# Kernel tuning notes

Measured on AMD Instinct MI355X. Metric: run time of the kernel, lower is better.

## Reference

```python
import jax, jax.numpy as jnp
import numpy as np

N = 100000      # nodes
E = 1600000     # edges (before self-loops)
IN_DIM = 128
HID = 32
HEADS = 4
EMB = 128
SLOPE = 0.2     # PyG GATConv default negative_slope


def setup_inputs() -> dict:
    key = jax.random.key(0)
    ks = jax.random.split(key, 16)
    def glorot(k, shape):
        fan_in = shape[0] if len(shape) > 1 else shape[-1]
        return jax.random.normal(k, shape, jnp.float32) * (1.0 / np.sqrt(fan_in))
    x = jax.random.normal(ks[0], (N, IN_DIM), jnp.float32)
    edge_index = jax.random.randint(ks[1], (2, E), 0, N)
    return {
        "x": x,
        "edge_index": edge_index,
        # layer 1: in_dim -> hidden (heads=4, concat)
        "W1": glorot(ks[2], (IN_DIM, HEADS * HID)),
        "att_src1": glorot(ks[3], (HEADS, HID)),
        "att_dst1": glorot(ks[4], (HEADS, HID)),
        "b1": jnp.zeros((HEADS * HID,), jnp.float32),
        # layer 2: hidden*heads -> hidden (heads=4, concat)
        "W2": glorot(ks[5], (HEADS * HID, HEADS * HID)),
        "att_src2": glorot(ks[6], (HEADS, HID)),
        "att_dst2": glorot(ks[7], (HEADS, HID)),
        "b2": jnp.zeros((HEADS * HID,), jnp.float32),
        # layer 3: hidden*heads -> embed (heads=1)
        "W3": glorot(ks[8], (HEADS * HID, EMB)),
        "att_src3": glorot(ks[9], (1, EMB)),
        "att_dst3": glorot(ks[10], (1, EMB)),
        "b3": jnp.zeros((EMB,), jnp.float32),
    }


def gat_conv(x, src, dst, W, att_src, att_dst, b, heads, out_ch):
    """One PyG-style GATConv (concat=True). src/dst already include self-loops."""
    n = x.shape[0]
    h = (x @ W).reshape(n, heads, out_ch)                 # [N,H,C]
    a_s = jnp.einsum('nhc,hc->nh', h, att_src)            # [N,H]
    a_d = jnp.einsum('nhc,hc->nh', h, att_dst)            # [N,H]
    e = jax.nn.leaky_relu(a_s[src] + a_d[dst], SLOPE)     # [E',H]
    # numerically stable softmax over irregular incoming neighborhoods (per dst)
    m = jax.ops.segment_max(e, dst, num_segments=n)       # [N,H]
    ex = jnp.exp(e - m[dst])
    denom = jax.ops.segment_sum(ex, dst, num_segments=n)  # [N,H]
    alpha = ex / denom[dst]                                # [E',H]
    out = jax.ops.segment_sum(h[src] * alpha[:, :, None], dst, num_segments=n)
    return out.reshape(n, heads * out_ch) + b


def reference(x, edge_index, W1, att_src1, att_dst1, b1,
              W2, att_src2, att_dst2, b2, W3, att_src3, att_dst3, b3):
    n = x.shape[0]
    loops = jnp.arange(n, dtype=edge_index.dtype)
    src = jnp.concatenate([edge_index[0], loops])  # PyG add_self_loops=True
    dst = jnp.concatenate([edge_index[1], loops])
    h = gat_conv(x, src, dst, W1, att_src1, att_dst1, b1, HEADS, HID)
    h = jax.nn.elu(h)
    h = gat_conv(h, src, dst, W2, att_src2, att_dst2, b2, HEADS, HID)
    h = jax.nn.elu(h)
    out = gat_conv(h, src, dst, W3, att_src3, att_dst3, b3, 1, EMB)
    return out
```

## Files before the change

### kernel.cpp

```cpp
#include <hip/hip_runtime.h>
#include <hip/hip_fp16.h>
#include <math.h>

#define N_NODES 100000
#define N_EDGES 1600000
#define SLOPE 0.2f

#define BSHIFT 8
#define NB 391
#define CHUNK 8192

typedef _Float16 f16x8 __attribute__((ext_vector_type(8)));
typedef float f32x4 __attribute__((ext_vector_type(4)));

__global__ __launch_bounds__(256) void partA1(const int* __restrict__ ei,
                                              int* __restrict__ bucket_count,
                                              int E, int n) {
  __shared__ int cnt[NB];
  for (int i = threadIdx.x; i < NB; i += 256) cnt[i] = 0;
  __syncthreads();
  int base = blockIdx.x * CHUNK;
  int total = E + n;
  int lim = min(base + CHUNK, total);
  for (int e = base + threadIdx.x; e < lim; e += 256) {
    int d = (e < E) ? ei[E + e] : (e - E);
    atomicAdd(&cnt[d >> BSHIFT], 1);
  }
  __syncthreads();
  for (int i = threadIdx.x; i < NB; i += 256)
    if (cnt[i]) atomicAdd(&bucket_count[i], cnt[i]);
}

__global__ __launch_bounds__(512) void scan_nb(
    const int* __restrict__ bucket_count, int* __restrict__ bucket_base,
    int* __restrict__ bucket_cursor) {
  __shared__ int lds[512];
  int t = threadIdx.x;
  int v = (t < NB) ? bucket_count[t] : 0;
  int x = v;
  lds[t] = x;
  __syncthreads();
  for (int off = 1; off < 512; off <<= 1) {
    int y = (t >= off) ? lds[t - off] : 0;
    __syncthreads();
    x += y;
    lds[t] = x;
    __syncthreads();
  }
  int excl = x - v;
  if (t <= NB) bucket_base[t] = excl;
  if (t < NB) bucket_cursor[t] = excl;
}

__global__ __launch_bounds__(256) void partA2(const int* __restrict__ ei,
                                              int* __restrict__ bucket_cursor,
                                              unsigned* __restrict__ part,
                                              int E, int n) {
  __shared__ int cnt[NB];
  __shared__ int res[NB];
  for (int i = threadIdx.x; i < NB; i += 256) cnt[i] = 0;
  __syncthreads();
  int base = blockIdx.x * CHUNK;
  int total = E + n;
  int lim = min(base + CHUNK, total);
  for (int e = base + threadIdx.x; e < lim; e += 256) {
    int d = (e < E) ? ei[E + e] : (e - E);
    atomicAdd(&cnt[d >> BSHIFT], 1);
  }
  __syncthreads();
  for (int i = threadIdx.x; i < NB; i += 256)
    res[i] = cnt[i] ? atomicAdd(&bucket_cursor[i], cnt[i]) : 0;
  __syncthreads();
  for (int e = base + threadIdx.x; e < lim; e += 256) {
    int s, d;
    if (e < E) { s = ei[e]; d = ei[E + e]; } else { s = d = e - E; }
    int b = d >> BSHIFT;
    int pos = atomicAdd(&res[b], 1);
    part[pos] = ((unsigned)s << BSHIFT) | (unsigned)(d & 255);
  }
}

__global__ __launch_bounds__(256) void passB(const unsigned* __restrict__ part,
                                             const int* __restrict__ bucket_base,
                                             int* __restrict__ row_start,
                                             int* __restrict__ edge_src, int n) {
  __shared__ int cnt[256];
  __shared__ int sc[256];
  __shared__ int loff[256];
  int b = blockIdx.x;
  int t = threadIdx.x;
  int node0 = b << BSHIFT;
  int bstart = bucket_base[b], bend = bucket_base[b + 1];
  cnt[t] = 0;
  __syncthreads();
  for (int i = bstart + t; i < bend; i += 256)
    atomicAdd(&cnt[part[i] & 255], 1);
  __syncthreads();
  int v = cnt[t];
  int x = v;
  sc[t] = x;
  __syncthreads();
  for (int off = 1; off < 256; off <<= 1) {
    int y = (t >= off) ? sc[t - off] : 0;
    __syncthreads();
    x += y;
    sc[t] = x;
    __syncthreads();
  }
  int excl = x - v;
  loff[t] = excl;
  int node = node0 + t;
  if (node < n) row_start[node] = bstart + excl;
  if (b == NB - 1 && t == 0) row_start[n] = bucket_base[NB];
  __syncthreads();
  for (int i = bstart + t; i < bend; i += 256) {
    unsigned p = part[i];
    int dl = p & 255;
    int pos = bstart + atomicAdd(&loff[dl], 1);
    edge_src[pos] = (int)(p >> BSHIFT);
  }
}

__global__ __launch_bounds__(256) void convert_w(
    const float* __restrict__ W1, const float* __restrict__ W2,
    const float* __restrict__ W3, __half* __restrict__ Wt1,
    __half* __restrict__ Wt2, __half* __restrict__ Wt3) {
  int idx = blockIdx.x * 256 + threadIdx.x;
  if (idx >= 3 * 16384) return;
  int mat = idx >> 14;
  int r = idx & 16383;
  int k = r >> 7, col = r & 127;
  const float* W = (mat == 0) ? W1 : (mat == 1) ? W2 : W3;
  __half* Wt = (mat == 0) ? Wt1 : (mat == 1) ? Wt2 : Wt3;
  Wt[col * 128 + k] = __float2half(W[k * 128 + col]);
}

template <int H>
__global__ __launch_bounds__(256) void gemm_att_mfma(
    const float* __restrict__ X, const __half* __restrict__ Wt,
    const float* __restrict__ att_src, const float* __restrict__ att_dst,
    __half* __restrict__ Y, float* __restrict__ a_s, float* __restrict__ a_d,
    int n) {
  __shared__ _Float16 A_lds[64 * 128];
  __shared__ _Float16 B_lds[128 * 128];
  int t = threadIdx.x;
  int r0 = blockIdx.x * 64;

  {
    int row = t >> 2;
    int c0 = (t & 3) * 32;
    const float* xp = X + (size_t)(r0 + row) * 128 + c0;
    bool inb = (r0 + row) < n;
#pragma unroll
    for (int i = 0; i < 8; i++) {
      float4 v;
      if (inb) v = *(const float4*)(xp + i * 4);
      else v = make_float4(0.f, 0.f, 0.f, 0.f);
      union { float2 f; __half2 h2[2]; } u;
      u.h2[0] = __floats2half2_rn(v.x, v.y);
      u.h2[1] = __floats2half2_rn(v.z, v.w);
      *(float2*)&A_lds[row * 128 + c0 + i * 4] = u.f;
    }
  }
  {
    const __half* wp = Wt + t * 64;
#pragma unroll
    for (int i = 0; i < 8; i++)
      *(float4*)&B_lds[t * 64 + i * 8] = *(const float4*)(wp + i * 8);
  }
  __syncthreads();

  int wv = t >> 6, lane = t & 63, quad = lane >> 4, l15 = lane & 15;
  const _Float16* Arow = &A_lds[(wv * 16 + l15) * 128];
  f32x4 acc[8];
#pragma unroll
  for (int ct = 0; ct < 8; ct++) acc[ct] = (f32x4){0.f, 0.f, 0.f, 0.f};

#pragma unroll
  for (int kb = 0; kb < 4; kb++) {
    f16x8 a = *(const f16x8*)(Arow + kb * 32 + quad * 8);
#pragma unroll
    for (int ct = 0; ct < 8; ct++) {
      f16x8 b = *(const f16x8*)(&B_lds[(ct * 16 + l15) * 128 + kb * 32 + quad * 8]);
      acc[ct] = __builtin_amdgcn_mfma_f32_16x16x32_f16(a, b, acc[ct], 0, 0, 0);
    }
  }

  int rbase = r0 + wv * 16 + quad * 4;
#pragma unroll
  for (int reg = 0; reg < 4; reg++) {
    int row = rbase + reg;
    if (row < n) {
#pragma unroll
      for (int ct = 0; ct < 8; ct++)
        Y[(size_t)row * 128 + ct * 16 + l15] = __float2half(acc[ct][reg]);
    }
  }

  float avs[8], avd[8];
#pragma unroll
  for (int ct = 0; ct < 8; ct++) {
    avs[ct] = att_src[ct * 16 + l15];
    avd[ct] = att_dst[ct * 16 + l15];
  }
  if constexpr (H == 4) {
    float ps[4][4], pd_[4][4];
#pragma unroll
    for (int hd = 0; hd < 4; hd++)
#pragma unroll
      for (int reg = 0; reg < 4; reg++) { ps[hd][reg] = 0.f; pd_[hd][reg] = 0.f; }
#pragma unroll
    for (int ct = 0; ct < 8; ct++) {
      int hd = ct >> 1;
#pragma unroll
      for (int reg = 0; reg < 4; reg++) {
        ps[hd][reg] = fmaf(acc[ct][reg], avs[ct], ps[hd][reg]);
        pd_[hd][reg] = fmaf(acc[ct][reg], avd[ct], pd_[hd][reg]);
      }
    }
#pragma unroll
    for (int off = 1; off <= 8; off <<= 1)
#pragma unroll
      for (int hd = 0; hd < 4; hd++)
#pragma unroll
        for (int reg = 0; reg < 4; reg++) {
          ps[hd][reg] += __shfl_xor(ps[hd][reg], off, 64);
          pd_[hd][reg] += __shfl_xor(pd_[hd][reg], off, 64);
        }
#pragma unroll
    for (int hd = 0; hd < 4; hd++)
      if (l15 == hd) {
#pragma unroll
        for (int reg = 0; reg < 4; reg++) {
          int row = rbase + reg;
          if (row < n) {
            a_s[row * 4 + hd] = ps[hd][reg];
            a_d[row * 4 + hd] = pd_[hd][reg];
          }
        }
      }
  } else {
    float ps[4] = {}, pd_[4] = {};
#pragma unroll
    for (int ct = 0; ct < 8; ct++)
#pragma unroll
      for (int reg = 0; reg < 4; reg++) {
        ps[reg] = fmaf(acc[ct][reg], avs[ct], ps[reg]);
        pd_[reg] = fmaf(acc[ct][reg], avd[ct], pd_[reg]);
      }
#pragma unroll
    for (int off = 1; off <= 8; off <<= 1)
#pragma unroll
      for (int reg = 0; reg < 4; reg++) {
        ps[reg] += __shfl_xor(ps[reg], off, 64);
        pd_[reg] += __shfl_xor(pd_[reg], off, 64);
      }
    if (l15 == 0) {
#pragma unroll
      for (int reg = 0; reg < 4; reg++) {
        int row = rbase + reg;
        if (row < n) { a_s[row] = ps[reg]; a_d[row] = pd_[reg]; }
      }
    }
  }
}

template <int H, bool DO_ELU>
__global__ __launch_bounds__(256) void agg_kernel(
    const __half* __restrict__ h, const float* __restrict__ a_s,
    const float* __restrict__ a_d, const int* __restrict__ row_start,
    const int* __restrict__ edge_src, const float* __restrict__ bias,
    float* __restrict__ out, int n) {
  const int C = 128 / H;
  __shared__ float w_lds[4][H * 66];
  __shared__ int sn_lds[4][64];
  int wslot = threadIdx.x >> 6;
  int wid = (blockIdx.x * blockDim.x + threadIdx.x) >> 6;
  int lane = threadIdx.x & 63;
  if (wid >= n) return;
  int start = row_start[wid], end = row_start[wid + 1];
  int deg = end - start;

  float adv[H];
#pragma unroll
  for (int hh = 0; hh < H; hh++) adv[hh] = a_d[wid * H + hh];

  if (deg <= 64) {
    bool valid = lane < deg;
    int sn = valid ? edge_src[start + lane] : 0;
    float e[H];
    if (valid) {
      if constexpr (H == 4) {
        float4 asv = *(const float4*)(a_s + (size_t)sn * 4);
        float t0 = asv.x + adv[0];
        float t1 = asv.y + adv[1];
        float t2 = asv.z + adv[2];
        float t3 = asv.w + adv[3];
        e[0] = t0 >= 0.f ? t0 : SLOPE * t0;
        e[1] = t1 >= 0.f ? t1 : SLOPE * t1;
        e[2] = t2 >= 0.f ? t2 : SLOPE * t2;
        e[3] = t3 >= 0.f ? t3 : SLOPE * t3;
      } else {
        float tt = a_s[sn] + adv[0];
        e[0] = tt >= 0.f ? tt : SLOPE * tt;
      }
    } else {
#pragma unroll
      for (int hh = 0; hh < H; hh++) e[hh] = -1e30f;
    }
    bool small = (deg <= 32);
    float m[H], w[H], s[H];
#pragma unroll
    for (int hh = 0; hh < H; hh++) m[hh] = e[hh];
#pragma unroll
    for (int off = 1; off <= 16; off <<= 1)
#pragma unroll
      for (int hh = 0; hh < H; hh++)
        m[hh] = fmaxf(m[hh], __shfl_xor(m[hh], off, 64));
    if (!small)
#pragma unroll
      for (int hh = 0; hh < H; hh++)
        m[hh] = fmaxf(m[hh], __shfl_xor(m[hh], 32, 64));
#pragma unroll
    for (int hh = 0; hh < H; hh++) {
      w[hh] = valid ? __expf(e[hh] - m[hh]) : 0.f;
      s[hh] = w[hh];
    }
#pragma unroll
    for (int off = 1; off <= 16; off <<= 1)
#pragma unroll
      for (int hh = 0; hh < H; hh++) s[hh] += __shfl_xor(s[hh], off, 64);
    if (!small)
#pragma unroll
      for (int hh = 0; hh < H; hh++) s[hh] += __shfl_xor(s[hh], 32, 64);
    sn_lds[wslot][lane] = sn;
#pragma unroll
    for (int hh = 0; hh < H; hh++)
      w_lds[wslot][hh * 66 + lane] = valid ? w[hh] * (1.f / s[hh]) : 0.f;
    __builtin_amdgcn_wave_barrier();

    int g = lane >> 5, l = lane & 31;
    int d0 = l * 4;
    int headBase = (H == 4) ? (l >> 3) * 66 : 0;
    float acc0 = 0.f, acc1 = 0.f, acc2 = 0.f, acc3 = 0.f;
    int degp4 = (deg + 3) & ~3;
    for (int eidx = g; eidx < degp4; eidx += 4) {
#pragma unroll
      for (int jj = 0; jj < 2; jj++) {
        int ei2 = eidx + jj * 2;
        int sn2 = sn_lds[wslot][ei2];
        float wv = w_lds[wslot][headBase + ei2];
        union { float2 f; __half2 h2[2]; } u;
        u.f = *(const float2*)(h + (size_t)sn2 * 128 + d0);
        float2 p0 = __half22float2(u.h2[0]);
        float2 p1 = __half22float2(u.h2[1]);
        acc0 = fmaf(p0.x, wv, acc0);
        acc1 = fmaf(p0.y, wv, acc1);
        acc2 = fmaf(p1.x, wv, acc2);
        acc3 = fmaf(p1.y, wv, acc3);
      }
    }
    acc0 += __shfl_xor(acc0, 32, 64);
    acc1 += __shfl_xor(acc1, 32, 64);
    acc2 += __shfl_xor(acc2, 32, 64);
    acc3 += __shfl_xor(acc3, 32, 64);
    if (lane < 32) {
      float4 bv = *(const float4*)(bias + d0);
      float o0 = acc0 + bv.x, o1 = acc1 + bv.y;
      float o2 = acc2 + bv.z, o3 = acc3 + bv.w;
      if (DO_ELU) {
        o0 = (o0 > 0.f) ? o0 : __expf(o0) - 1.f;
        o1 = (o1 > 0.f) ? o1 : __expf(o1) - 1.f;
        o2 = (o2 > 0.f) ? o2 : __expf(o2) - 1.f;
        o3 = (o3 > 0.f) ? o3 : __expf(o3) - 1.f;
      }
      float4 ov = {o0, o1, o2, o3};
      *(float4*)(out + (size_t)wid * 128 + d0) = ov;
    }
    return;
  }

  {
    const int G = C / 2;
    int head = lane / G;
    float m[H], s[H];
#pragma unroll
    for (int hh = 0; hh < H; hh++) { m[hh] = -1e30f; s[hh] = 0.f; }
    for (int idx = start + lane; idx < end; idx += 64) {
      int sn = edge_src[idx];
#pragma unroll
      for (int hh = 0; hh < H; hh++) {
        float e = a_s[sn * H + hh] + adv[hh];
        e = (e >= 0.f) ? e : SLOPE * e;
        float mn = fmaxf(m[hh], e);
        s[hh] = s[hh] * __expf(m[hh] - mn) + __expf(e - mn);
        m[hh] = mn;
      }
    }
    for (int off = 1; off < 64; off <<= 1) {
#pragma unroll
      for (int hh = 0; hh < H; hh++) {
        float mo = __shfl_xor(m[hh], off, 64);
        float so = __shfl_xor(s[hh], off, 64);
        float mn = fmaxf(m[hh], mo);
        s[hh] = s[hh] * __expf(m[hh] - mn) + so * __expf(mo - mn);
        m[hh] = mn;
      }
    }
    int d0 = lane * 2;
    float mh = m[head];
    float rsh = 1.f / s[head];
    float adh = adv[head];
    float acc0 = 0.f, acc1 = 0.f;
    for (int idx = start; idx < end; idx++) {
      int sn = edge_src[idx];
      float e = a_s[sn * H + head] + adh;
      e = (e >= 0.f) ? e : SLOPE * e;
      float w = __expf(e - mh) * rsh;
      float2 hv = __half22float2(*(const __half2*)(h + (size_t)sn * 128 + d0));
      acc0 += w * hv.x;
      acc1 += w * hv.y;
    }
    float o0 = acc0 + bias[d0];
    float o1 = acc1 + bias[d0 + 1];
    if (DO_ELU) {
      o0 = (o0 > 0.f) ? o0 : __expf(o0) - 1.f;
      o1 = (o1 > 0.f) ? o1 : __expf(o1) - 1.f;
    }
    out[(size_t)wid * 128 + d0] = o0;
    out[(size_t)wid * 128 + d0 + 1] = o1;
  }
}

extern "C" void kernel_launch(void* const* d_in, const int* in_sizes, int n_in,
                              void* d_out, int out_size, void* d_ws,
                              size_t ws_size, hipStream_t stream) {
  const float* x = (const float*)d_in[0];
  const int* ei = (const int*)d_in[1];
  const float* W1 = (const float*)d_in[2];
  const float* as1 = (const float*)d_in[3];
  const float* ad1 = (const float*)d_in[4];
  const float* b1 = (const float*)d_in[5];
  const float* W2 = (const float*)d_in[6];
  const float* as2 = (const float*)d_in[7];
  const float* ad2 = (const float*)d_in[8];
  const float* b2 = (const float*)d_in[9];
  const float* W3 = (const float*)d_in[10];
  const float* as3 = (const float*)d_in[11];
  const float* ad3 = (const float*)d_in[12];
  const float* b3 = (const float*)d_in[13];
  float* out = (float*)d_out;

  const int n = N_NODES, E = N_EDGES, total = E + n;

  char* ws = (char*)d_ws;
  size_t off = 0;
  auto alloc = [&](size_t bytes) -> char* {
    char* p = ws + off;
    off = (off + bytes + 255) & ~(size_t)255;
    return p;
  };
  __half* hbuf = (__half*)alloc(sizeof(__half) * (size_t)n * 128);
  float* a_s = (float*)alloc(sizeof(float) * n * 4);
  float* a_d = (float*)alloc(sizeof(float) * n * 4);
  unsigned* part = (unsigned*)alloc(sizeof(unsigned) * total);
  int* edge_src = (int*)alloc(sizeof(int) * total);
  int* row_start = (int*)alloc(sizeof(int) * (n + 1));
  int* bucket_count = (int*)alloc(sizeof(int) * (NB + 1));
  int* bucket_base = (int*)alloc(sizeof(int) * (NB + 1));
  int* bucket_cursor = (int*)alloc(sizeof(int) * (NB + 1));
  __half* Wt1 = (__half*)alloc(sizeof(__half) * 16384);
  __half* Wt2 = (__half*)alloc(sizeof(__half) * 16384);
  __half* Wt3 = (__half*)alloc(sizeof(__half) * 16384);

  hipMemsetAsync(bucket_count, 0, sizeof(int) * (NB + 1), stream);

  convert_w<<<192, 256, 0, stream>>>(W1, W2, W3, Wt1, Wt2, Wt3);

  int nblkA = (total + CHUNK - 1) / CHUNK;
  partA1<<<nblkA, 256, 0, stream>>>(ei, bucket_count, E, n);
  scan_nb<<<1, 512, 0, stream>>>(bucket_count, bucket_base, bucket_cursor);
  partA2<<<nblkA, 256, 0, stream>>>(ei, bucket_cursor, part, E, n);
  passB<<<NB, 256, 0, stream>>>(part, bucket_base, row_start, edge_src, n);

  int agg_blocks = (n + 3) / 4;
  int gemm_blocks = (n + 63) / 64;

  gemm_att_mfma<4><<<gemm_blocks, 256, 0, stream>>>(x, Wt1, as1, ad1, hbuf,
                                                    a_s, a_d, n);
  agg_kernel<4, true><<<agg_blocks, 256, 0, stream>>>(
      hbuf, a_s, a_d, row_start, edge_src, b1, out, n);

  gemm_att_mfma<4><<<gemm_blocks, 256, 0, stream>>>(out, Wt2, as2, ad2, hbuf,
                                                    a_s, a_d, n);
  agg_kernel<4, true><<<agg_blocks, 256, 0, stream>>>(
      hbuf, a_s, a_d, row_start, edge_src, b2, out, n);

  gemm_att_mfma<1><<<gemm_blocks, 256, 0, stream>>>(out, Wt3, as3, ad3, hbuf,
                                                    a_s, a_d, n);
  agg_kernel<1, false><<<agg_blocks, 256, 0, stream>>>(
      hbuf, a_s, a_d, row_start, edge_src, b3, out, n);
}
```

Baseline: 522.0 us.

## Process two nodes per wavefront in GAT aggregation with 16-byte gathers

The aggregation kernel now assigns two destination nodes to each 64-lane wavefront, each half-wave handling one node's softmax over up to 32 neighbors, with a wave-uniform fallback to the serial path when either node has degree above 32. The gather phase uses 16 lanes per node loading 8 halfs (16 bytes) per edge instead of 4, with two edge groups per node reduced by a shuffle. This aims to cut idle lanes for average degree ~17 and halve wave count, at the cost of more registers and a slower fallback when any paired node exceeds 32 neighbors.

```diff
diff --git a/kernel.cpp b/kernel.cpp
--- a/kernel.cpp
+++ b/kernel.cpp
@@ -277,17 +277,30 @@
   int wslot = threadIdx.x >> 6;
   int wid = (blockIdx.x * blockDim.x + threadIdx.x) >> 6;
   int lane = threadIdx.x & 63;
-  if (wid >= n) return;
-  int start = row_start[wid], end = row_start[wid + 1];
+  int nPairs = (n + 1) >> 1;
+  if (wid >= nPairs) return;
+
+  int sub = lane >> 5, sl = lane & 31;
+  int node = wid * 2 + sub;
+  bool nodeValid = node < n;
+  int start = 0, end = 0;
+  if (nodeValid) { start = row_start[node]; end = row_start[node + 1]; }
   int deg = end - start;
 
-  float adv[H];
-#pragma unroll
-  for (int hh = 0; hh < H; hh++) adv[hh] = a_d[wid * H + hh];
-
-  if (deg <= 64) {
-    bool valid = lane < deg;
-    int sn = valid ? edge_src[start + lane] : 0;
+  if (__all(deg <= 32)) {
+    float adv[H];
+#pragma unroll
+    for (int hh = 0; hh < H; hh++) adv[hh] = 0.f;
+    if (nodeValid) {
+      if constexpr (H == 4) {
+        float4 av = *(const float4*)(a_d + (size_t)node * 4);
+        adv[0] = av.x; adv[1] = av.y; adv[2] = av.z; adv[3] = av.w;
+      } else {
+        adv[0] = a_d[node];
+      }
+    }
+    bool valid = sl < deg;
+    int sn = valid ? edge_src[start + sl] : 0;
     float e[H];
     if (valid) {
       if constexpr (H == 4) {
@@ -308,7 +321,6 @@
 #pragma unroll
       for (int hh = 0; hh < H; hh++) e[hh] = -1e30f;
     }
-    bool small = (deg <= 32);
     float m[H], w[H], s[H];
 #pragma unroll
     for (int hh = 0; hh < H; hh++) m[hh] = e[hh];
@@ -317,10 +329,6 @@
 #pragma unroll
       for (int hh = 0; hh < H; hh++)
         m[hh] = fmaxf(m[hh], __shfl_xor(m[hh], off, 64));
-    if (!small)
-#pragma unroll
-      for (int hh = 0; hh < H; hh++)
-        m[hh] = fmaxf(m[hh], __shfl_xor(m[hh], 32, 64));
 #pragma unroll
     for (int hh = 0; hh < H; hh++) {
       w[hh] = valid ? __expf(e[hh] - m[hh]) : 0.f;
@@ -330,67 +338,81 @@
     for (int off = 1; off <= 16; off <<= 1)
 #pragma unroll
       for (int hh = 0; hh < H; hh++) s[hh] += __shfl_xor(s[hh], off, 64);
-    if (!small)
-#pragma unroll
-      for (int hh = 0; hh < H; hh++) s[hh] += __shfl_xor(s[hh], 32, 64);
-    sn_lds[wslot][lane] = sn;
+    sn_lds[wslot][sub * 32 + sl] = sn;
 #pragma unroll
     for (int hh = 0; hh < H; hh++)
-      w_lds[wslot][hh * 66 + lane] = valid ? w[hh] * (1.f / s[hh]) : 0.f;
+      w_lds[wslot][hh * 66 + sub * 33 + sl] = valid ? w[hh] * (1.f / s[hh]) : 0.f;
     __builtin_amdgcn_wave_barrier();
 
-    int g = lane >> 5, l = lane & 31;
-    int d0 = l * 4;
-    int headBase = (H == 4) ? (l >> 3) * 66 : 0;
-    float acc0 = 0.f, acc1 = 0.f, acc2 = 0.f, acc3 = 0.f;
-    int degp4 = (deg + 3) & ~3;
-    for (int eidx = g; eidx < degp4; eidx += 4) {
-#pragma unroll
-      for (int jj = 0; jj < 2; jj++) {
+    int g = (lane >> 4) & 1, l = lane & 15;
+    int d0 = l * 8;
+    int wOff = ((H == 4) ? (l >> 2) * 66 : 0) + sub * 33;
+    float acc[8];
+#pragma unroll
+    for (int k = 0; k < 8; k++) acc[k] = 0.f;
+    int degp8 = (deg + 7) & ~7;
+    for (int eidx = g; eidx < degp8; eidx += 8) {
+#pragma unroll
+      for (int jj = 0; jj < 4; jj++) {
         int ei2 = eidx + jj * 2;
-        int sn2 = sn_lds[wslot][ei2];
-        float wv = w_lds[wslot][headBase + ei2];
-        union { float2 f; __half2 h2[2]; } u;
-        u.f = *(const float2*)(h + (size_t)sn2 * 128 + d0);
+        int sn2 = sn_lds[wslot][sub * 32 + ei2];
+        float wv = w_lds[wslot][wOff + ei2];
+        union { float4 f; __half2 h2[4]; } u;
+        u.f = *(const float4*)(h + (size_t)sn2 * 128 + d0);
         float2 p0 = __half22float2(u.h2[0]);
         float2 p1 = __half22float2(u.h2[1]);
-        acc0 = fmaf(p0.x, wv, acc0);
-        acc1 = fmaf(p0.y, wv, acc1);
-        acc2 = fmaf(p1.x, wv, acc2);
-        acc3 = fmaf(p1.y, wv, acc3);
-      }
-    }
-    acc0 += __shfl_xor(acc0, 32, 64);
-    acc1 += __shfl_xor(acc1, 32, 64);
-    acc2 += __shfl_xor(acc2, 32, 64);
-    acc3 += __shfl_xor(acc3, 32, 64);
-    if (lane < 32) {
-      float4 bv = *(const float4*)(bias + d0);
-      float o0 = acc0 + bv.x, o1 = acc1 + bv.y;
-      float o2 = acc2 + bv.z, o3 = acc3 + bv.w;
+        float2 p2 = __half22float2(u.h2[2]);
+        float2 p3 = __half22float2(u.h2[3]);
+        acc[0] = fmaf(p0.x, wv, acc[0]);
+        acc[1] = fmaf(p0.y, wv, acc[1]);
+        acc[2] = fmaf(p1.x, wv, acc[2]);
+        acc[3] = fmaf(p1.y, wv, acc[3]);
+        acc[4] = fmaf(p2.x, wv, acc[4]);
+        acc[5] = fmaf(p2.y, wv, acc[5]);
+        acc[6] = fmaf(p3.x, wv, acc[6]);
+        acc[7] = fmaf(p3.y, wv, acc[7]);
+      }
+    }
+#pragma unroll
+    for (int k = 0; k < 8; k++) acc[k] += __shfl_xor(acc[k], 16, 64);
+    if ((lane & 16) == 0 && nodeValid) {
+      float4 bv0 = *(const float4*)(bias + d0);
+      float4 bv1 = *(const float4*)(bias + d0 + 4);
+      float o[8];
+      o[0] = acc[0] + bv0.x; o[1] = acc[1] + bv0.y;
+      o[2] = acc[2] + bv0.z; o[3] = acc[3] + bv0.w;
+      o[4] = acc[4] + bv1.x; o[5] = acc[5] + bv1.y;
+      o[6] = acc[6] + bv1.z; o[7] = acc[7] + bv1.w;
       if (DO_ELU) {
-        o0 = (o0 > 0.f) ? o0 : __expf(o0) - 1.f;
-        o1 = (o1 > 0.f) ? o1 : __expf(o1) - 1.f;
-        o2 = (o2 > 0.f) ? o2 : __expf(o2) - 1.f;
-        o3 = (o3 > 0.f) ? o3 : __expf(o3) - 1.f;
-      }
-      float4 ov = {o0, o1, o2, o3};
-      *(float4*)(out + (size_t)wid * 128 + d0) = ov;
+#pragma unroll
+        for (int k = 0; k < 8; k++)
+          o[k] = (o[k] > 0.f) ? o[k] : __expf(o[k]) - 1.f;
+      }
+      float4 ov0 = {o[0], o[1], o[2], o[3]};
+      float4 ov1 = {o[4], o[5], o[6], o[7]};
+      *(float4*)(out + (size_t)node * 128 + d0) = ov0;
+      *(float4*)(out + (size_t)node * 128 + d0 + 4) = ov1;
     }
     return;
   }
 
-  {
+  for (int s2 = 0; s2 < 2; s2++) {
+    int nd = wid * 2 + s2;
+    if (nd >= n) break;
+    int st = row_start[nd], en = row_start[nd + 1];
+    float advn[H];
+#pragma unroll
+    for (int hh = 0; hh < H; hh++) advn[hh] = a_d[nd * H + hh];
     const int G = C / 2;
     int head = lane / G;
     float m[H], s[H];
 #pragma unroll
     for (int hh = 0; hh < H; hh++) { m[hh] = -1e30f; s[hh] = 0.f; }
-    for (int idx = start + lane; idx < end; idx += 64) {
+    for (int idx = st + lane; idx < en; idx += 64) {
       int sn = edge_src[idx];
 #pragma unroll
       for (int hh = 0; hh < H; hh++) {
-        float e = a_s[sn * H + hh] + adv[hh];
+        float e = a_s[sn * H + hh] + advn[hh];
         e = (e >= 0.f) ? e : SLOPE * e;
         float mn = fmaxf(m[hh], e);
         s[hh] = s[hh] * __expf(m[hh] - mn) + __expf(e - mn);
@@ -410,9 +432,9 @@
     int d0 = lane * 2;
     float mh = m[head];
     float rsh = 1.f / s[head];
-    float adh = adv[head];
+    float adh = advn[head];
     float acc0 = 0.f, acc1 = 0.f;
-    for (int idx = start; idx < end; idx++) {
+    for (int idx = st; idx < en; idx++) {
       int sn = edge_src[idx];
       float e = a_s[sn * H + head] + adh;
       e = (e >= 0.f) ? e : SLOPE * e;
@@ -427,8 +449,8 @@
       o0 = (o0 > 0.f) ? o0 : __expf(o0) - 1.f;
       o1 = (o1 > 0.f) ? o1 : __expf(o1) - 1.f;
     }
-    out[(size_t)wid * 128 + d0] = o0;
-    out[(size_t)wid * 128 + d0 + 1] = o1;
+    out[(size_t)nd * 128 + d0] = o0;
+    out[(size_t)nd * 128 + d0 + 1] = o1;
   }
 }
 
@@ -483,7 +505,8 @@
   partA2<<<nblkA, 256, 0, stream>>>(ei, bucket_cursor, part, E, n);
   passB<<<NB, 256, 0, stream>>>(part, bucket_base, row_start, edge_src, n);
 
-  int agg_blocks = (n + 3) / 4;
+  int nPairs = (n + 1) / 2;
+  int agg_blocks = (nPairs + 3) / 4;
   int gemm_blocks = (n + 63) / 64;
 
   gemm_att_mfma<4><<<gemm_blocks, 256, 0, stream>>>(x, Wt1, as1, ad1, hbuf,
```

Result: slower. 551.3 us (+5.6%).
